# Kernel optimization log

Hardware: AMD Instinct MI355X
Metric: run time of the kernel (lower is better)

Reference implementation:

```python
import jax, jax.numpy as jnp
import numpy as np


def _lstm(x, Wih, Whh, bih, bhh):
    """PyTorch-convention single-layer LSTM. x: [B,T,D] -> outputs [B,T,H], h_T [B,H]."""
    B = x.shape[0]
    H = Whh.shape[1]
    # precompute input projections for all timesteps: [T,B,4H]
    xg = jnp.einsum('btd,gd->tbg', x, Wih) + (bih + bhh)

    def step(carry, xt):
        h, c = carry
        gates = xt + h @ Whh.T  # [B,4H]
        i, f, g, o = jnp.split(gates, 4, axis=-1)
        i = jax.nn.sigmoid(i)
        f = jax.nn.sigmoid(f)
        g = jnp.tanh(g)
        o = jax.nn.sigmoid(o)
        c = f * c + i * g
        h = o * jnp.tanh(c)
        return (h, c), h

    h0 = jnp.zeros((B, H), dtype=x.dtype)
    c0 = jnp.zeros((B, H), dtype=x.dtype)
    (hT, _), hs = jax.lax.scan(step, (h0, c0), xg)
    return jnp.transpose(hs, (1, 0, 2)), hT


def setup_inputs() -> dict:
    key = jax.random.key(0)
    ks = jax.random.split(key, 13)
    B, T, D, H1, H2 = 32768, 60, 7, 64, 32
    s = lambda k, shape, fan: jax.random.normal(k, shape, jnp.float32) * (1.0 / np.sqrt(fan))
    return {
        'x': jax.random.normal(ks[0], (B, T, D), jnp.float32),
        'Wih1': s(ks[1], (4 * H1, D), H1),
        'Whh1': s(ks[2], (4 * H1, H1), H1),
        'bih1': s(ks[3], (4 * H1,), H1),
        'bhh1': s(ks[4], (4 * H1,), H1),
        'Wih2': s(ks[5], (4 * H2, H1), H2),
        'Whh2': s(ks[6], (4 * H2, H2), H2),
        'bih2': s(ks[7], (4 * H2,), H2),
        'bhh2': s(ks[8], (4 * H2,), H2),
        'Wd': s(ks[9], (16, H2), H2),
        'bd': s(ks[10], (16,), H2),
        'Wo': s(ks[11], (1, 16), 16),
        'bo': s(ks[12], (1,), 16),
    }


def reference(x, Wih1, Whh1, bih1, bhh1, Wih2, Whh2, bih2, bhh2, Wd, bd, Wo, bo):
    out1, _ = _lstm(x, Wih1, Whh1, bih1, bhh1)        # [B,60,64]
    _, hT = _lstm(out1, Wih2, Whh2, bih2, bhh2)       # h_n[-1]: [B,32]
    dense = jax.nn.relu(hT @ Wd.T + bd)               # [B,16]
    return jax.nn.sigmoid(dense @ Wo.T + bo)          # [B,1]
```

## Files before the change

kernel.cpp:

```cpp
#include <hip/hip_runtime.h>


using f32x16 = __attribute__((ext_vector_type(16))) float;
using s16x8  = __attribute__((ext_vector_type(8)))  short;
using uint2v = __attribute__((ext_vector_type(2)))  unsigned int;
typedef unsigned int uint;
typedef unsigned short ushort;

#define THREADS 512
#define NBLOCKS 1024
#define L2E 1.44269504f

__device__ __forceinline__ float fsig(float v) {
    float e = __builtin_amdgcn_exp2f(-L2E * v);
    return __builtin_amdgcn_rcpf(1.0f + e);
}
__device__ __forceinline__ void lstm_act_pre(float zi, float zf, float zg, float zo,
                                             float& cs, float& hv) {
    float ei = __builtin_amdgcn_exp2f(zi);
    float ef = __builtin_amdgcn_exp2f(zf);
    float eg = __builtin_amdgcn_exp2f(zg);
    float eo = __builtin_amdgcn_exp2f(zo);
    float ai = 1.0f + ei, af = 1.0f + ef;
    float r0 = __builtin_amdgcn_rcpf(ai * af);
    float iv = r0 * af, fv = r0 * ai;
    float ag = 1.0f + eg, ao = 1.0f + eo;
    float r1 = __builtin_amdgcn_rcpf(ag * ao);
    float gv = __builtin_fmaf(-2.0f * r1, ao, 1.0f);
    float ov = r1 * ag;
    float c = __builtin_fmaf(fv, cs, iv * gv);
    cs = c;
    float et = __builtin_amdgcn_exp2f((2.0f * L2E) * c);
    float tt = __builtin_fmaf(-2.0f, __builtin_amdgcn_rcpf(1.0f + et), 1.0f);
    hv = ov * tt;
}
__device__ __forceinline__ ushort bfhi(float w) {
    uint u = __builtin_bit_cast(uint, w);
    return (ushort)((u + 0x7fffu + ((u >> 16) & 1u)) >> 16);
}
__device__ __forceinline__ uint pkbf(float a, float b) {
    uint r;
    asm("v_cvt_pk_bf16_f32 %0, %1, %2" : "=v"(r) : "v"(a), "v"(b));
    return r;
}
__device__ __forceinline__ uint4 pack8(const ushort v[8]) {
    return make_uint4(v[0] | ((uint)v[1] << 16), v[2] | ((uint)v[3] << 16),
                      v[4] | ((uint)v[5] << 16), v[6] | ((uint)v[7] << 16));
}
#define MFMA32(a, b, c) \
    __builtin_amdgcn_mfma_f32_32x32x16_bf16(__builtin_bit_cast(s16x8, (a)), \
        __builtin_bit_cast(s16x8, (b)), (c), 0, 0, 0)
#define PLSWAP(a, b) __builtin_amdgcn_permlane32_swap((a), (b), false, false)

__global__ void __launch_bounds__(THREADS, 4) lstm_kernel(
    const float* __restrict__ x,
    const float* __restrict__ Wih1, const float* __restrict__ Whh1,
    const float* __restrict__ bih1, const float* __restrict__ bhh1,
    const float* __restrict__ Wih2, const float* __restrict__ Whh2,
    const float* __restrict__ bih2, const float* __restrict__ bhh2,
    const float* __restrict__ Wd, const float* __restrict__ bd,
    const float* __restrict__ Wo, const float* __restrict__ bo,
    float* __restrict__ out)
{
    __shared__ uint4 sH1[2][4][64];
    __shared__ uint4 sH2q[2][32][4];
    __shared__ uint4 sX[2][32];
    __shared__ float sWd[512];
    __shared__ float sBd[16], sWo[16], sBo[1];
    __shared__ float sHs[1024];

    const int tid = threadIdx.x;
    const int lane = tid & 63, wave = tid >> 6;
    const int hh = lane >> 5, n = lane & 31;
    const int bbase = blockIdx.x * 32;

    for (int i = tid; i < 512; i += THREADS) sWd[i] = Wd[i];
    if (tid < 16) { sBd[tid] = bd[tid]; sWo[tid] = Wo[tid]; }
    if (tid == 0) sBo[0] = bo[0];
    {
        uint4 z = make_uint4(0, 0, 0, 0);
        uint4* p1 = &sH1[0][0][0];
        for (int i = tid; i < 512; i += THREADS) p1[i] = z;
        uint4* p2 = &sH2q[0][0][0];
        for (int i = tid; i < 256; i += THREADS) p2[i] = z;
    }

    if (wave < 4) {
        const int w = wave;
        uint4 wr[8];
        uint4 xwf[2];
#pragma unroll
        for (int m = 0; m < 2; ++m) {
            int gate = 2 * m + (n >> 4);
            int G = gate * 64 + 16 * w + (n & 15);
            float sc = (gate == 2) ? (2.0f * L2E) : (-L2E);
#pragma unroll
            for (int kt = 0; kt < 4; ++kt) {
                const float* src = Whh1 + G * 64 + kt * 16 + hh * 8;
                ushort v[8];
#pragma unroll
                for (int e = 0; e < 8; ++e) v[e] = bfhi(src[e] * sc);
                wr[m * 4 + kt] = pack8(v);
            }
            float b1 = (bih1[G] + bhh1[G]) * sc;
            ushort v[8];
#pragma unroll
            for (int e = 0; e < 8; ++e)
                v[e] = (hh == 0) ? bfhi(((e < 7) ? Wih1[G * 7 + e] * sc : b1)) : (ushort)0;
            xwf[m] = pack8(v);
        }
        float cst[8];
#pragma unroll
        for (int r = 0; r < 8; ++r) cst[r] = 0.f;
        __syncthreads();

        f32x16 Z;
#pragma unroll
        for (int i = 0; i < 16; ++i) Z[i] = 0.f;

        for (int t = 0; t < 60; ++t) {
            const int rp = (t + 1) & 1;
            uint4 xB = sX[t & 1][n];
            uint4 h0 = sH1[rp][0][lane];
            uint4 h1f = sH1[rp][1][lane];
            uint4 h2f = sH1[rp][2][lane];
            uint4 h3 = sH1[rp][3][lane];
            f32x16 cA = MFMA32(xwf[0], xB, Z);
            f32x16 cB = MFMA32(xwf[1], xB, Z);
            cA = MFMA32(wr[0], h0, cA);  cB = MFMA32(wr[4], h0, cB);
            cA = MFMA32(wr[1], h1f, cA); cB = MFMA32(wr[5], h1f, cB);
            cA = MFMA32(wr[2], h2f, cA); cB = MFMA32(wr[6], h2f, cB);
            cA = MFMA32(wr[3], h3, cA);  cB = MFMA32(wr[7], h3, cB);
            float hv[8];
#pragma unroll
            for (int r = 0; r < 8; ++r)
                lstm_act_pre(cA[r], cA[r + 8], cB[r], cB[r + 8], cst[r], hv[r]);
            uint Q00 = pkbf(hv[0], hv[1]), Q01 = pkbf(hv[4], hv[5]);
            uint Q10 = pkbf(hv[2], hv[3]), Q11 = pkbf(hv[6], hv[7]);
            uint2v sA = PLSWAP(Q00, Q01);
            uint2v sB = PLSWAP(Q10, Q11);
            sH1[t & 1][w][lane] = make_uint4(sA[0], sB[0], sA[1], sB[1]);
            __syncthreads();
        }
        __syncthreads();
    } else {
        const int w2 = wave - 4;
        uint4 wih[4], whh[2];
        f32x16 bias2;
        {
            int gate = n >> 3;
            int G = gate * 32 + 8 * w2 + (n & 7);
            float sc = (gate == 2) ? (2.0f * L2E) : (-L2E);
#pragma unroll
            for (int kt = 0; kt < 4; ++kt) {
                const float* src = Wih2 + G * 64 + kt * 16 + hh * 8;
                ushort v[8];
#pragma unroll
                for (int e = 0; e < 8; ++e) v[e] = bfhi(src[e] * sc);
                wih[kt] = pack8(v);
            }
#pragma unroll
            for (int kt = 0; kt < 2; ++kt) {
                const float* src = Whh2 + G * 32 + kt * 16 + hh * 8;
                ushort v[8];
#pragma unroll
                for (int e = 0; e < 8; ++e) v[e] = bfhi(src[e] * sc);
                whh[kt] = pack8(v);
            }
#pragma unroll
            for (int r = 0; r < 16; ++r) {
                int row = (r & 3) + 8 * (r >> 2) + 4 * hh;
                int Gb = (row >> 3) * 32 + 8 * w2 + (row & 7);
                float scb = ((row >> 3) == 2) ? (2.0f * L2E) : (-L2E);
                bias2[r] = (bih2[Gb] + bhh2[Gb]) * scb;
            }
        }
        float cst[4];
#pragma unroll
        for (int s = 0; s < 4; ++s) cst[s] = 0.f;
        float hv[4];
        const float* xp = x + (size_t)(bbase + lane) * 420;
        const bool xload = (wave == 4) && (lane < 32);
        if (xload) {
            float x0[7];
#pragma unroll
            for (int d = 0; d < 7; ++d) x0[d] = xp[d];
            sX[0][lane] = make_uint4(pkbf(x0[0], x0[1]), pkbf(x0[2], x0[3]),
                                     pkbf(x0[4], x0[5]), pkbf(x0[6], 1.0f));
        }
        __syncthreads();

        for (int t = 0; t < 60; ++t) {
            float xr[7];
            if (xload && t < 59) {
#pragma unroll
                for (int d = 0; d < 7; ++d) xr[d] = xp[(t + 1) * 7 + d];
            }
            if (t > 0) {
                const int rp = (t + 1) & 1;
                uint4 h0 = sH1[rp][0][lane];
                uint4 h1f = sH1[rp][1][lane];
                uint4 h2f = sH1[rp][2][lane];
                uint4 h3 = sH1[rp][3][lane];
                uint4 g0 = sH2q[t & 1][n][hh];
                uint4 g1 = sH2q[t & 1][n][2 + hh];
                f32x16 c = bias2;
                c = MFMA32(wih[0], h0, c);
                c = MFMA32(wih[1], h1f, c);
                c = MFMA32(wih[2], h2f, c);
                c = MFMA32(wih[3], h3, c);
                c = MFMA32(whh[0], g0, c);
                c = MFMA32(whh[1], g1, c);
#pragma unroll
                for (int s = 0; s < 4; ++s)
                    lstm_act_pre(c[s], c[s + 4], c[s + 8], c[s + 12], cst[s], hv[s]);
                uint Qe = pkbf(hv[0], hv[1]), Qf = pkbf(hv[2], hv[3]);
                uint* p = (uint*)&sH2q[rp][n][0];
                *(uint2*)&p[4 * w2 + 2 * hh] = make_uint2(Qe, Qf);
            }
            if (xload && t < 59) {
                sX[(t + 1) & 1][lane] = make_uint4(pkbf(xr[0], xr[1]), pkbf(xr[2], xr[3]),
                                                   pkbf(xr[4], xr[5]), pkbf(xr[6], 1.0f));
            }
            __syncthreads();
        }
        {
            uint4 h0 = sH1[1][0][lane];
            uint4 h1f = sH1[1][1][lane];
            uint4 h2f = sH1[1][2][lane];
            uint4 h3 = sH1[1][3][lane];
            uint4 g0 = sH2q[0][n][hh];
            uint4 g1 = sH2q[0][n][2 + hh];
            f32x16 c = bias2;
            c = MFMA32(wih[0], h0, c);
            c = MFMA32(wih[1], h1f, c);
            c = MFMA32(wih[2], h2f, c);
            c = MFMA32(wih[3], h3, c);
            c = MFMA32(whh[0], g0, c);
            c = MFMA32(whh[1], g1, c);
#pragma unroll
            for (int s = 0; s < 4; ++s)
                lstm_act_pre(c[s], c[s + 4], c[s + 8], c[s + 12], cst[s], hv[s]);
#pragma unroll
            for (int s = 0; s < 4; ++s)
                sHs[n * 32 + 8 * w2 + 4 * hh + s] = hv[s];
        }
        __syncthreads();

        if (wave == 4 && lane < 32) {
            const float* hcol = sHs + lane * 32;
            float a[16];
#pragma unroll
            for (int o = 0; o < 16; ++o) a[o] = sBd[o];
#pragma unroll 4
            for (int u = 0; u < 32; ++u) {
                float hvv = hcol[u];
#pragma unroll
                for (int o = 0; o < 16; ++o)
                    a[o] = __builtin_fmaf(sWd[o * 32 + u], hvv, a[o]);
            }
            float rr = sBo[0];
#pragma unroll
            for (int o = 0; o < 16; ++o)
                rr = __builtin_fmaf(sWo[o], fmaxf(a[o], 0.0f), rr);
            out[bbase + lane] = fsig(rr);
        }
    }
}

extern "C" void kernel_launch(void* const* d_in, const int* in_sizes, int n_in,
                              void* d_out, int out_size, void* d_ws, size_t ws_size,
                              hipStream_t stream) {
    const float* x    = (const float*)d_in[0];
    const float* Wih1 = (const float*)d_in[1];
    const float* Whh1 = (const float*)d_in[2];
    const float* bih1 = (const float*)d_in[3];
    const float* bhh1 = (const float*)d_in[4];
    const float* Wih2 = (const float*)d_in[5];
    const float* Whh2 = (const float*)d_in[6];
    const float* bih2 = (const float*)d_in[7];
    const float* bhh2 = (const float*)d_in[8];
    const float* Wd   = (const float*)d_in[9];
    const float* bd   = (const float*)d_in[10];
    const float* Wo   = (const float*)d_in[11];
    const float* bo   = (const float*)d_in[12];
    float* out = (float*)d_out;

    lstm_kernel<<<NBLOCKS, THREADS, 0, stream>>>(
        x, Wih1, Whh1, bih1, bhh1, Wih2, Whh2, bih2, bhh2, Wd, bd, Wo, bo, out);
}
```

Baseline: 307.8 us.

## Repartition LSTM work into two waves each computing both layers with register-held own state

Shrinks the block from eight waves (four for layer 1, four for layer 2) to two waves. Each wave computes half of the layer-1 and half of the layer-2 hidden units. Each wave keeps its own half of h in registers and reads only the partner's half from shared memory, with the weight K-order permuted so its own half comes first. This is meant to cut barrier cost and shared-memory traffic and to load-balance the two layers. The trade-off is a much heavier per-wave instruction load and higher register pressure: the layer-1 Whh weights are held in registers and the input-projection weights move to LDS.

```diff
diff --git a/kernel.cpp b/kernel.cpp
--- a/kernel.cpp
+++ b/kernel.cpp
@@ -7,7 +7,7 @@
 typedef unsigned int uint;
 typedef unsigned short ushort;
 
-#define THREADS 512
+#define THREADS 128
 #define NBLOCKS 1024
 #define L2E 1.44269504f
 
@@ -52,7 +52,7 @@
         __builtin_bit_cast(s16x8, (b)), (c), 0, 0, 0)
 #define PLSWAP(a, b) __builtin_amdgcn_permlane32_swap((a), (b), false, false)
 
-__global__ void __launch_bounds__(THREADS, 4) lstm_kernel(
+__global__ void __launch_bounds__(THREADS, 2) lstm_kernel(
     const float* __restrict__ x,
     const float* __restrict__ Wih1, const float* __restrict__ Whh1,
     const float* __restrict__ bih1, const float* __restrict__ bhh1,
@@ -63,14 +63,17 @@
     float* __restrict__ out)
 {
     __shared__ uint4 sH1[2][4][64];
-    __shared__ uint4 sH2q[2][32][4];
+    __shared__ uint4 sH2[2][2][64];
+    __shared__ uint4 sXW[2][4][64];
     __shared__ uint4 sX[2][32];
+    __shared__ float sB2[2][2][32];
     __shared__ float sWd[512];
     __shared__ float sBd[16], sWo[16], sBo[1];
     __shared__ float sHs[1024];
 
     const int tid = threadIdx.x;
-    const int lane = tid & 63, wave = tid >> 6;
+    const int lane = tid & 63;
+    const int W = tid >> 6;
     const int hh = lane >> 5, n = lane & 31;
     const int bbase = blockIdx.x * 32;
 
@@ -79,192 +82,199 @@
     if (tid == 0) sBo[0] = bo[0];
     {
         uint4 z = make_uint4(0, 0, 0, 0);
-        uint4* p1 = &sH1[0][0][0];
-        for (int i = tid; i < 512; i += THREADS) p1[i] = z;
-        uint4* p2 = &sH2q[0][0][0];
-        for (int i = tid; i < 256; i += THREADS) p2[i] = z;
-    }
-
-    if (wave < 4) {
-        const int w = wave;
-        uint4 wr[8];
-        uint4 xwf[2];
-#pragma unroll
-        for (int m = 0; m < 2; ++m) {
-            int gate = 2 * m + (n >> 4);
-            int G = gate * 64 + 16 * w + (n & 15);
-            float sc = (gate == 2) ? (2.0f * L2E) : (-L2E);
-#pragma unroll
-            for (int kt = 0; kt < 4; ++kt) {
-                const float* src = Whh1 + G * 64 + kt * 16 + hh * 8;
-                ushort v[8];
-#pragma unroll
-                for (int e = 0; e < 8; ++e) v[e] = bfhi(src[e] * sc);
-                wr[m * 4 + kt] = pack8(v);
-            }
-            float b1 = (bih1[G] + bhh1[G]) * sc;
+        uint4* p1 = &sH1[1][0][0];
+        for (int i = tid; i < 256; i += THREADS) p1[i] = z;
+        uint4* p2 = &sH2[1][0][0];
+        for (int i = tid; i < 128; i += THREADS) p2[i] = z;
+    }
+
+    const int gate = n >> 3, u3 = n & 7;
+    const float sc = (gate == 2) ? (2.0f * L2E) : (-L2E);
+
+    uint4 whh1[4][4], wih2[2][4], whh2[2][2];
+#pragma unroll
+    for (int m = 0; m < 4; ++m) {
+        int G = gate * 64 + 32 * W + 8 * m + u3;
+#pragma unroll
+        for (int j = 0; j < 4; ++j) {
+            int kt = j ^ (2 * W);
+            const float* src = Whh1 + G * 64 + kt * 16 + hh * 8;
             ushort v[8];
 #pragma unroll
-            for (int e = 0; e < 8; ++e)
-                v[e] = (hh == 0) ? bfhi(((e < 7) ? Wih1[G * 7 + e] * sc : b1)) : (ushort)0;
-            xwf[m] = pack8(v);
-        }
-        float cst[8];
-#pragma unroll
-        for (int r = 0; r < 8; ++r) cst[r] = 0.f;
+            for (int e = 0; e < 8; ++e) v[e] = bfhi(src[e] * sc);
+            whh1[m][j] = pack8(v);
+        }
+        float b1 = (bih1[G] + bhh1[G]) * sc;
+        ushort v[8];
+#pragma unroll
+        for (int e = 0; e < 8; ++e)
+            v[e] = (hh == 0) ? bfhi((e < 7) ? Wih1[G * 7 + e] * sc : b1) : (ushort)0;
+        sXW[W][m][lane] = pack8(v);
+    }
+#pragma unroll
+    for (int mm = 0; mm < 2; ++mm) {
+        int G = gate * 32 + 16 * W + 8 * mm + u3;
+#pragma unroll
+        for (int j = 0; j < 4; ++j) {
+            int kt = j ^ (2 * W);
+            const float* src = Wih2 + G * 64 + kt * 16 + hh * 8;
+            ushort v[8];
+#pragma unroll
+            for (int e = 0; e < 8; ++e) v[e] = bfhi(src[e] * sc);
+            wih2[mm][j] = pack8(v);
+        }
+#pragma unroll
+        for (int j = 0; j < 2; ++j) {
+            int kt = j ^ W;
+            const float* src = Whh2 + G * 32 + kt * 16 + hh * 8;
+            ushort v[8];
+#pragma unroll
+            for (int e = 0; e < 8; ++e) v[e] = bfhi(src[e] * sc);
+            whh2[mm][j] = pack8(v);
+        }
+        if (hh == 0) sB2[W][mm][n] = (bih2[G] + bhh2[G]) * sc;
+    }
+
+    const float* xp = x + (size_t)(bbase + lane) * 420;
+    if (W == 1 && lane < 32) {
+        float x0[7];
+#pragma unroll
+        for (int d = 0; d < 7; ++d) x0[d] = xp[d];
+        sX[0][lane] = make_uint4(pkbf(x0[0], x0[1]), pkbf(x0[2], x0[3]),
+                                 pkbf(x0[4], x0[5]), pkbf(x0[6], 1.0f));
+    }
+
+    float c1[16], c2[8];
+#pragma unroll
+    for (int i = 0; i < 16; ++i) c1[i] = 0.f;
+#pragma unroll
+    for (int i = 0; i < 8; ++i) c2[i] = 0.f;
+    uint4 h1o0 = make_uint4(0, 0, 0, 0), h1o1 = make_uint4(0, 0, 0, 0);
+    uint4 h2o = make_uint4(0, 0, 0, 0);
+    float h2v[2][4];
+    const int pW = 2 * (1 - W);
+
+    __syncthreads();
+
+    auto l2body = [&](uint4 h1p0, uint4 h1p1, uint4 h2p) {
+#pragma unroll
+        for (int mm = 0; mm < 2; ++mm) {
+            float4 b0 = *(const float4*)&sB2[W][mm][4 * hh + 0];
+            float4 b1q = *(const float4*)&sB2[W][mm][4 * hh + 8];
+            float4 b2q = *(const float4*)&sB2[W][mm][4 * hh + 16];
+            float4 b3q = *(const float4*)&sB2[W][mm][4 * hh + 24];
+            f32x16 c;
+            c[0] = b0.x;  c[1] = b0.y;  c[2] = b0.z;  c[3] = b0.w;
+            c[4] = b1q.x; c[5] = b1q.y; c[6] = b1q.z; c[7] = b1q.w;
+            c[8] = b2q.x; c[9] = b2q.y; c[10] = b2q.z; c[11] = b2q.w;
+            c[12] = b3q.x; c[13] = b3q.y; c[14] = b3q.z; c[15] = b3q.w;
+            c = MFMA32(wih2[mm][0], h1o0, c);
+            c = MFMA32(wih2[mm][1], h1o1, c);
+            c = MFMA32(wih2[mm][2], h1p0, c);
+            c = MFMA32(wih2[mm][3], h1p1, c);
+            c = MFMA32(whh2[mm][0], h2o, c);
+            c = MFMA32(whh2[mm][1], h2p, c);
+#pragma unroll
+            for (int s = 0; s < 4; ++s)
+                lstm_act_pre(c[s], c[s + 4], c[s + 8], c[s + 12],
+                             c2[mm * 4 + s], h2v[mm][s]);
+        }
+    };
+
+    for (int t = 0; t < 60; ++t) {
+        const int pr = (t + 1) & 1;
+        uint4 h1p0 = sH1[pr][pW + 0][lane];
+        uint4 h1p1 = sH1[pr][pW + 1][lane];
+        uint4 xB = sX[t & 1][n];
+
+        if (t > 0) {
+            uint4 h2p = sH2[t & 1][1 - W][lane];
+            l2body(h1p0, h1p1, h2p);
+            uint Pa = pkbf(h2v[0][0], h2v[0][1]);
+            uint Pb = pkbf(h2v[1][0], h2v[1][1]);
+            uint Pc = pkbf(h2v[0][2], h2v[0][3]);
+            uint Pd = pkbf(h2v[1][2], h2v[1][3]);
+            uint2v sA = PLSWAP(Pa, Pb);
+            uint2v sB = PLSWAP(Pc, Pd);
+            h2o = make_uint4(sA[0], sB[0], sA[1], sB[1]);
+            sH2[pr][W][lane] = h2o;
+        }
+
+        float xr[7];
+        if (W == 1 && lane < 32 && t < 59) {
+#pragma unroll
+            for (int d = 0; d < 7; ++d) xr[d] = xp[(t + 1) * 7 + d];
+        }
+
+        uint P0[4], P1[4];
+#pragma unroll
+        for (int m = 0; m < 4; ++m) {
+            uint4 xw = sXW[W][m][lane];
+            f32x16 c;
+#pragma unroll
+            for (int i = 0; i < 16; ++i) c[i] = 0.f;
+            c = MFMA32(whh1[m][0], h1o0, c);
+            c = MFMA32(whh1[m][1], h1o1, c);
+            c = MFMA32(whh1[m][2], h1p0, c);
+            c = MFMA32(whh1[m][3], h1p1, c);
+            c = MFMA32(xw, xB, c);
+            float hv0, hv1, hv2, hv3;
+            lstm_act_pre(c[0], c[4], c[8],  c[12], c1[m * 4 + 0], hv0);
+            lstm_act_pre(c[1], c[5], c[9],  c[13], c1[m * 4 + 1], hv1);
+            lstm_act_pre(c[2], c[6], c[10], c[14], c1[m * 4 + 2], hv2);
+            lstm_act_pre(c[3], c[7], c[11], c[15], c1[m * 4 + 3], hv3);
+            P0[m] = pkbf(hv0, hv1);
+            P1[m] = pkbf(hv2, hv3);
+        }
+        {
+            uint2v sA = PLSWAP(P0[0], P0[1]);
+            uint2v sB = PLSWAP(P1[0], P1[1]);
+            h1o0 = make_uint4(sA[0], sB[0], sA[1], sB[1]);
+            sH1[t & 1][2 * W + 0][lane] = h1o0;
+        }
+        {
+            uint2v sA = PLSWAP(P0[2], P0[3]);
+            uint2v sB = PLSWAP(P1[2], P1[3]);
+            h1o1 = make_uint4(sA[0], sB[0], sA[1], sB[1]);
+            sH1[t & 1][2 * W + 1][lane] = h1o1;
+        }
+        if (W == 1 && lane < 32 && t < 59) {
+            sX[pr][lane] = make_uint4(pkbf(xr[0], xr[1]), pkbf(xr[2], xr[3]),
+                                      pkbf(xr[4], xr[5]), pkbf(xr[6], 1.0f));
+        }
         __syncthreads();
-
-        f32x16 Z;
-#pragma unroll
-        for (int i = 0; i < 16; ++i) Z[i] = 0.f;
-
-        for (int t = 0; t < 60; ++t) {
-            const int rp = (t + 1) & 1;
-            uint4 xB = sX[t & 1][n];
-            uint4 h0 = sH1[rp][0][lane];
-            uint4 h1f = sH1[rp][1][lane];
-            uint4 h2f = sH1[rp][2][lane];
-            uint4 h3 = sH1[rp][3][lane];
-            f32x16 cA = MFMA32(xwf[0], xB, Z);
-            f32x16 cB = MFMA32(xwf[1], xB, Z);
-            cA = MFMA32(wr[0], h0, cA);  cB = MFMA32(wr[4], h0, cB);
-            cA = MFMA32(wr[1], h1f, cA); cB = MFMA32(wr[5], h1f, cB);
-            cA = MFMA32(wr[2], h2f, cA); cB = MFMA32(wr[6], h2f, cB);
-            cA = MFMA32(wr[3], h3, cA);  cB = MFMA32(wr[7], h3, cB);
-            float hv[8];
-#pragma unroll
-            for (int r = 0; r < 8; ++r)
-                lstm_act_pre(cA[r], cA[r + 8], cB[r], cB[r + 8], cst[r], hv[r]);
-            uint Q00 = pkbf(hv[0], hv[1]), Q01 = pkbf(hv[4], hv[5]);
-            uint Q10 = pkbf(hv[2], hv[3]), Q11 = pkbf(hv[6], hv[7]);
-            uint2v sA = PLSWAP(Q00, Q01);
-            uint2v sB = PLSWAP(Q10, Q11);
-            sH1[t & 1][w][lane] = make_uint4(sA[0], sB[0], sA[1], sB[1]);
-            __syncthreads();
-        }
-        __syncthreads();
-    } else {
-        const int w2 = wave - 4;
-        uint4 wih[4], whh[2];
-        f32x16 bias2;
-        {
-            int gate = n >> 3;
-            int G = gate * 32 + 8 * w2 + (n & 7);
-            float sc = (gate == 2) ? (2.0f * L2E) : (-L2E);
-#pragma unroll
-            for (int kt = 0; kt < 4; ++kt) {
-                const float* src = Wih2 + G * 64 + kt * 16 + hh * 8;
-                ushort v[8];
-#pragma unroll
-                for (int e = 0; e < 8; ++e) v[e] = bfhi(src[e] * sc);
-                wih[kt] = pack8(v);
-            }
-#pragma unroll
-            for (int kt = 0; kt < 2; ++kt) {
-                const float* src = Whh2 + G * 32 + kt * 16 + hh * 8;
-                ushort v[8];
-#pragma unroll
-                for (int e = 0; e < 8; ++e) v[e] = bfhi(src[e] * sc);
-                whh[kt] = pack8(v);
-            }
-#pragma unroll
-            for (int r = 0; r < 16; ++r) {
-                int row = (r & 3) + 8 * (r >> 2) + 4 * hh;
-                int Gb = (row >> 3) * 32 + 8 * w2 + (row & 7);
-                float scb = ((row >> 3) == 2) ? (2.0f * L2E) : (-L2E);
-                bias2[r] = (bih2[Gb] + bhh2[Gb]) * scb;
-            }
-        }
-        float cst[4];
-#pragma unroll
-        for (int s = 0; s < 4; ++s) cst[s] = 0.f;
-        float hv[4];
-        const float* xp = x + (size_t)(bbase + lane) * 420;
-        const bool xload = (wave == 4) && (lane < 32);
-        if (xload) {
-            float x0[7];
-#pragma unroll
-            for (int d = 0; d < 7; ++d) x0[d] = xp[d];
-            sX[0][lane] = make_uint4(pkbf(x0[0], x0[1]), pkbf(x0[2], x0[3]),
-                                     pkbf(x0[4], x0[5]), pkbf(x0[6], 1.0f));
-        }
-        __syncthreads();
-
-        for (int t = 0; t < 60; ++t) {
-            float xr[7];
-            if (xload && t < 59) {
-#pragma unroll
-                for (int d = 0; d < 7; ++d) xr[d] = xp[(t + 1) * 7 + d];
-            }
-            if (t > 0) {
-                const int rp = (t + 1) & 1;
-                uint4 h0 = sH1[rp][0][lane];
-                uint4 h1f = sH1[rp][1][lane];
-                uint4 h2f = sH1[rp][2][lane];
-                uint4 h3 = sH1[rp][3][lane];
-                uint4 g0 = sH2q[t & 1][n][hh];
-                uint4 g1 = sH2q[t & 1][n][2 + hh];
-                f32x16 c = bias2;
-                c = MFMA32(wih[0], h0, c);
-                c = MFMA32(wih[1], h1f, c);
-                c = MFMA32(wih[2], h2f, c);
-                c = MFMA32(wih[3], h3, c);
-                c = MFMA32(whh[0], g0, c);
-                c = MFMA32(whh[1], g1, c);
-#pragma unroll
-                for (int s = 0; s < 4; ++s)
-                    lstm_act_pre(c[s], c[s + 4], c[s + 8], c[s + 12], cst[s], hv[s]);
-                uint Qe = pkbf(hv[0], hv[1]), Qf = pkbf(hv[2], hv[3]);
-                uint* p = (uint*)&sH2q[rp][n][0];
-                *(uint2*)&p[4 * w2 + 2 * hh] = make_uint2(Qe, Qf);
-            }
-            if (xload && t < 59) {
-                sX[(t + 1) & 1][lane] = make_uint4(pkbf(xr[0], xr[1]), pkbf(xr[2], xr[3]),
-                                                   pkbf(xr[4], xr[5]), pkbf(xr[6], 1.0f));
-            }
-            __syncthreads();
-        }
-        {
-            uint4 h0 = sH1[1][0][lane];
-            uint4 h1f = sH1[1][1][lane];
-            uint4 h2f = sH1[1][2][lane];
-            uint4 h3 = sH1[1][3][lane];
-            uint4 g0 = sH2q[0][n][hh];
-            uint4 g1 = sH2q[0][n][2 + hh];
-            f32x16 c = bias2;
-            c = MFMA32(wih[0], h0, c);
-            c = MFMA32(wih[1], h1f, c);
-            c = MFMA32(wih[2], h2f, c);
-            c = MFMA32(wih[3], h3, c);
-            c = MFMA32(whh[0], g0, c);
-            c = MFMA32(whh[1], g1, c);
+    }
+
+    {
+        uint4 h1p0 = sH1[1][pW + 0][lane];
+        uint4 h1p1 = sH1[1][pW + 1][lane];
+        uint4 h2p = sH2[0][1 - W][lane];
+        l2body(h1p0, h1p1, h2p);
+#pragma unroll
+        for (int mm = 0; mm < 2; ++mm)
 #pragma unroll
             for (int s = 0; s < 4; ++s)
-                lstm_act_pre(c[s], c[s + 4], c[s + 8], c[s + 12], cst[s], hv[s]);
-#pragma unroll
-            for (int s = 0; s < 4; ++s)
-                sHs[n * 32 + 8 * w2 + 4 * hh + s] = hv[s];
-        }
-        __syncthreads();
-
-        if (wave == 4 && lane < 32) {
-            const float* hcol = sHs + lane * 32;
-            float a[16];
-#pragma unroll
-            for (int o = 0; o < 16; ++o) a[o] = sBd[o];
+                sHs[n * 32 + 16 * W + 8 * mm + 4 * hh + s] = h2v[mm][s];
+    }
+    __syncthreads();
+
+    if (W == 0 && lane < 32) {
+        const float* hcol = sHs + lane * 32;
+        float a[16];
+#pragma unroll
+        for (int o = 0; o < 16; ++o) a[o] = sBd[o];
 #pragma unroll 4
-            for (int u = 0; u < 32; ++u) {
-                float hvv = hcol[u];
-#pragma unroll
-                for (int o = 0; o < 16; ++o)
-                    a[o] = __builtin_fmaf(sWd[o * 32 + u], hvv, a[o]);
-            }
-            float rr = sBo[0];
+        for (int u = 0; u < 32; ++u) {
+            float hvv = hcol[u];
 #pragma unroll
             for (int o = 0; o < 16; ++o)
-                rr = __builtin_fmaf(sWo[o], fmaxf(a[o], 0.0f), rr);
-            out[bbase + lane] = fsig(rr);
-        }
+                a[o] = __builtin_fmaf(sWd[o * 32 + u], hvv, a[o]);
+        }
+        float rr = sBo[0];
+#pragma unroll
+        for (int o = 0; o < 16; ++o)
+            rr = __builtin_fmaf(sWo[o], fmaxf(a[o], 0.0f), rr);
+        out[bbase + lane] = fsig(rr);
     }
 }
 
```

Result: slower. 339.7 us (+10.4%).
